# Performance work log

Hardware: AMD Instinct MI355X
Metric: run time of the kernel (lower is better)

## Reference

```python
import jax, jax.numpy as jnp
import numpy as np
import math

B, S, DIM, H = 2, 2048, 1024, 16
Q_DIM = 64                 # cfg.pair_dim
V_DIM = Q_DIM * 3 // 2     # 96
MAX_POS = 2048             # cfg.rope_max_position
EPS = 1e-8
SOFTCAP = 5.0


def apply_rope(x):
    # x: [B, S, H, D]; faithful to torch version: freq = 1/logspace(0, log10(max_pos), D//2)
    D = x.shape[-1]
    nf = D // 2
    freq = 1.0 / jnp.logspace(0.0, math.log10(MAX_POS), nf, dtype=x.dtype)   # [nf]
    positions = jnp.arange(x.shape[1], dtype=x.dtype)                         # [S]
    theta = positions[:, None] * freq                                         # [S, nf]
    sin_t = jnp.sin(theta)[None, :, None, :]                                  # [1,S,1,nf]
    cos_t = jnp.cos(theta)[None, :, None, :]
    x1 = x[..., ::2]
    x2 = x[..., 1::2]
    return jnp.concatenate([x1 * cos_t - x2 * sin_t, x1 * sin_t + x2 * cos_t], axis=-1)


def setup_inputs() -> dict:
    key = jax.random.key(0)
    ks = jax.random.split(key, 9)
    x = jax.random.normal(ks[0], (B, S, DIM), dtype=jnp.float32)
    attention_bias = jax.random.normal(ks[1], (B, H, S, S), dtype=jnp.float32)
    rms_weight = jnp.ones((DIM,), dtype=jnp.float32)
    sd = 1.0 / math.sqrt(DIM)
    Wq = jax.random.normal(ks[2], (DIM, H * Q_DIM), dtype=jnp.float32) * sd
    Wk = jax.random.normal(ks[3], (DIM, Q_DIM), dtype=jnp.float32) * sd
    Wv = jax.random.normal(ks[4], (DIM, V_DIM), dtype=jnp.float32) * sd
    bv = jax.random.normal(ks[5], (V_DIM,), dtype=jnp.float32) * sd
    Wo = jax.random.normal(ks[6], (H * V_DIM, DIM), dtype=jnp.float32) / math.sqrt(H * V_DIM)
    bo = jax.random.normal(ks[7], (DIM,), dtype=jnp.float32) * sd
    return {"x": x, "attention_bias": attention_bias, "rms_weight": rms_weight,
            "Wq": Wq, "Wk": Wk, "Wv": Wv, "bv": bv, "Wo": Wo, "bo": bo}


def reference(x, attention_bias, rms_weight, Wq, Wk, Wv, bv, Wo, bo):
    # RMSNorm
    xn = x * rms_weight / jnp.sqrt(jnp.mean(x * x, axis=-1, keepdims=True) + EPS)
    # projections (MQA: single shared k and v head)
    q = (xn @ Wq).reshape(B, S, H, Q_DIM)          # [B,S,H,Dq]
    k = xn @ Wk                                     # [B,S,Dq]
    v = xn @ Wv + bv                                # [B,S,Dv]
    # RoPE
    q = apply_rope(q)
    k = apply_rope(k[:, :, None, :])[:, :, 0, :]
    # attention logits with tanh soft-cap and external bias: [B,H,S,S]
    logits = jnp.einsum('bihd,bjd->bhij', q, k)
    logits = jnp.tanh((logits + attention_bias) / SOFTCAP) * SOFTCAP
    attn = jax.nn.softmax(logits, axis=-1)
    # context: shared V across heads
    ctx = jnp.einsum('bhij,bjd->bihd', attn, v).reshape(B, S, H * V_DIM)
    return ctx @ Wo + bo
```

## Files before the change

kernel.cpp:

```cpp
#include <hip/hip_runtime.h>
#include <math.h>

#define B_   2
#define S_   2048
#define DIM_ 1024
#define H_   16
#define QD_  64
#define VD_  96
#define NQKV 1184
#define EPS_ 1e-8f

using half_t = _Float16;
using half8  = __attribute__((ext_vector_type(8))) _Float16;
using half4v = __attribute__((ext_vector_type(4))) _Float16;
using f32x4  = __attribute__((ext_vector_type(4))) float;

__global__ __launch_bounds__(256) void rmsnorm_h(const float* __restrict__ x,
                                                 const float* __restrict__ w,
                                                 half_t* __restrict__ xn) {
    int row = blockIdx.x;
    int t = threadIdx.x;
    float4 v = ((const float4*)(x + (size_t)row * DIM_))[t];
    float ss = v.x * v.x + v.y * v.y + v.z * v.z + v.w * v.w;
#pragma unroll
    for (int off = 32; off > 0; off >>= 1) ss += __shfl_down(ss, off, 64);
    __shared__ float wsum[4];
    if ((t & 63) == 0) wsum[t >> 6] = ss;
    __syncthreads();
    float tot = wsum[0] + wsum[1] + wsum[2] + wsum[3];
    float scale = rsqrtf(tot * (1.0f / DIM_) + EPS_);
    float4 wv = ((const float4*)w)[t];
    half4v o;
    o[0] = (half_t)(v.x * wv.x * scale);
    o[1] = (half_t)(v.y * wv.y * scale);
    o[2] = (half_t)(v.z * wv.z * scale);
    o[3] = (half_t)(v.w * wv.w * scale);
    ((half4v*)(xn + (size_t)row * DIM_))[t] = o;
}

template <typename TIN>
__global__ __launch_bounds__(256) void transpose_cvt(const TIN* __restrict__ in,
                                                     half_t* __restrict__ out,
                                                     int R, int C, int ldin,
                                                     size_t zin, size_t zout) {
    __shared__ float tile[32][33];
    in += (size_t)blockIdx.z * zin;
    out += (size_t)blockIdx.z * zout;
    int tx = threadIdx.x & 31, ty = threadIdx.x >> 5;
#pragma unroll
    for (int i = 0; i < 32; i += 8) {
        int r = blockIdx.y * 32 + ty + i, c = blockIdx.x * 32 + tx;
        tile[ty + i][tx] = (float)in[(size_t)r * ldin + c];
    }
    __syncthreads();
#pragma unroll
    for (int i = 0; i < 32; i += 8) {
        int orow = blockIdx.x * 32 + ty + i, ocol = blockIdx.y * 32 + tx;
        out[(size_t)orow * R + ocol] = (half_t)tile[tx][ty + i];
    }
}

__global__ __launch_bounds__(256) void fill_qkv_bias(const float* __restrict__ bv,
                                                     float* __restrict__ bq) {
    int i = blockIdx.x * 256 + threadIdx.x;
    if (i < NQKV) bq[i] = (i >= H_ * QD_ + QD_) ? bv[i - (H_ * QD_ + QD_)] : 0.0f;
}

template <typename OutT, bool BIAS>
__global__ __launch_bounds__(256) void gemm_h(const half_t* __restrict__ A,
                                              const half_t* __restrict__ BT,
                                              OutT* __restrict__ C,
                                              const float* __restrict__ bias,
                                              int M, int N, int K) {
    __shared__ half_t As[128][40];
    __shared__ half_t Bs[128][40];
    int t = threadIdx.x;
    int w = t >> 6, lane = t & 63, l15 = lane & 15, l4 = lane >> 4;
    int wm = (w >> 1) * 64, wn = (w & 1) * 64;
    int m0 = blockIdx.y * 128, n0 = blockIdx.x * 128;
    int r0 = t >> 2, off0 = (t & 3) * 8;
    f32x4 acc[4][4] = {};
    const half8 hz = {};

    const half_t* Ap0 = A + (size_t)(m0 + r0) * K + off0;
    const half_t* Ap1 = Ap0 + (size_t)64 * K;
    const half_t* Bp0 = BT + (size_t)(n0 + r0) * K + off0;
    const half_t* Bp1 = Bp0 + (size_t)64 * K;
    bool bok0 = (n0 + r0) < N, bok1 = (n0 + r0 + 64) < N;

    half8 a0 = *(const half8*)Ap0;
    half8 a1 = *(const half8*)Ap1;
    half8 b0 = bok0 ? *(const half8*)Bp0 : hz;
    half8 b1 = bok1 ? *(const half8*)Bp1 : hz;

    for (int k0 = 0; k0 < K; k0 += 32) {
        __syncthreads();
        *(half8*)&As[r0][off0] = a0;
        *(half8*)&As[r0 + 64][off0] = a1;
        *(half8*)&Bs[r0][off0] = b0;
        *(half8*)&Bs[r0 + 64][off0] = b1;
        __syncthreads();
        if (k0 + 32 < K) {
            a0 = *(const half8*)(Ap0 + k0 + 32);
            a1 = *(const half8*)(Ap1 + k0 + 32);
            b0 = bok0 ? *(const half8*)(Bp0 + k0 + 32) : hz;
            b1 = bok1 ? *(const half8*)(Bp1 + k0 + 32) : hz;
        }
        half8 af[4], bf[4];
#pragma unroll
        for (int mt = 0; mt < 4; ++mt) af[mt] = *(const half8*)&As[wm + mt * 16 + l15][l4 * 8];
#pragma unroll
        for (int nt = 0; nt < 4; ++nt) bf[nt] = *(const half8*)&Bs[wn + nt * 16 + l15][l4 * 8];
#pragma unroll
        for (int mt = 0; mt < 4; ++mt)
#pragma unroll
            for (int nt = 0; nt < 4; ++nt)
                acc[mt][nt] =
                    __builtin_amdgcn_mfma_f32_16x16x32_f16(af[mt], bf[nt], acc[mt][nt], 0, 0, 0);
    }

#pragma unroll
    for (int mt = 0; mt < 4; ++mt)
#pragma unroll
        for (int nt = 0; nt < 4; ++nt) {
            int n = n0 + wn + nt * 16 + l15;
            if (n < N) {
#pragma unroll
                for (int reg = 0; reg < 4; ++reg) {
                    int m = m0 + wm + mt * 16 + l4 * 4 + reg;
                    float v = acc[mt][nt][reg];
                    if (BIAS) v += bias[n];
                    C[(size_t)m * N + n] = (OutT)v;
                }
            }
        }
}

__global__ __launch_bounds__(256) void rope_h(const half_t* __restrict__ in, int ldin,
                                              half_t* __restrict__ out,
                                              int hc, int total_pairs) {
    int p = blockIdx.x * 256 + threadIdx.x;
    if (p >= total_pairs) return;
    int i = p & 31;
    int chunk = p >> 5;
    int row = chunk / hc;
    int h = chunk - row * hc;
    int s = row & (S_ - 1);
    const half_t* src = in + (size_t)row * ldin + h * 64 + 2 * i;
    float x1 = (float)src[0], x2 = (float)src[1];
    float freq = exp2f((float)i * (-11.0f / 31.0f));
    float th = (float)s * freq;
    float sn, cs;
    sincosf(th, &sn, &cs);
    half_t* dst = out + (size_t)chunk * 64;
    dst[i] = (half_t)(x1 * cs - x2 * sn);
    dst[i + 32] = (half_t)(x1 * sn + x2 * cs);
}

__global__ __launch_bounds__(256, 4) void attn_mfma(const half_t* __restrict__ qh,
                                                    const half_t* __restrict__ kh,
                                                    const half_t* __restrict__ vt,
                                                    const float* __restrict__ bias,
                                                    half_t* __restrict__ ctx) {
    __shared__ half_t ks[64][72];
    __shared__ half_t vs[96][72];
    __shared__ half_t ps[4][16][72];

    int t = threadIdx.x;
    int w = t >> 6, lane = t & 63, l15 = lane & 15, l4 = lane >> 4;
    int i0 = blockIdx.x * 64, h = blockIdx.y, b = blockIdx.z;

    const half_t* qbase =
        qh + (((size_t)(b * S_ + i0 + w * 16 + l15) * H_ + h) << 6) + l4 * 8;
    half8 qf0 = *(const half8*)qbase;
    half8 qf1 = *(const half8*)(qbase + 32);

    f32x4 cacc[6] = {};
    float rsum = 0.f;

    int sr = t >> 3, so = (t & 7) * 8;
    const float* bbase =
        bias + ((size_t)(b * H_ + h) * S_ + i0 + w * 16 + l15) * S_ + l4 * 4;
    const half_t* krow0 = kh + (((size_t)b * S_ + sr) << 6) + so;
    const half_t* krow1 = krow0 + ((size_t)32 << 6);
    const half_t* vrow0 = vt + ((size_t)b * 96 + sr) * S_ + so;
    const half_t* vrow1 = vrow0 + (size_t)32 * S_;
    const half_t* vrow2 = vrow0 + (size_t)64 * S_;

    half8 kr0, kr1, vr0, vr1, vr2;
    f32x4 bc[4], bn[4];

    kr0 = *(const half8*)krow0;
    kr1 = *(const half8*)krow1;
    vr0 = *(const half8*)vrow0;
    vr1 = *(const half8*)vrow1;
    vr2 = *(const half8*)vrow2;
#pragma unroll
    for (int nt = 0; nt < 4; ++nt) bc[nt] = *(const f32x4*)(bbase + nt * 16);

    *(half8*)&ks[sr][so] = kr0;
    *(half8*)&ks[sr + 32][so] = kr1;
    *(half8*)&vs[sr][so] = vr0;
    *(half8*)&vs[sr + 32][so] = vr1;
    *(half8*)&vs[sr + 64][so] = vr2;
    __syncthreads();

    for (int j0 = 0; j0 < S_; j0 += 64) {
        int jn = j0 + 64;
        bool more = jn < S_;

        if (more) {
            kr0 = *(const half8*)(krow0 + ((size_t)jn << 6));
            kr1 = *(const half8*)(krow1 + ((size_t)jn << 6));
            vr0 = *(const half8*)(vrow0 + jn);
            vr1 = *(const half8*)(vrow1 + jn);
            vr2 = *(const half8*)(vrow2 + jn);
#pragma unroll
            for (int nt = 0; nt < 4; ++nt) bn[nt] = *(const f32x4*)(bbase + jn + nt * 16);
        }

#pragma unroll
        for (int hf = 0; hf < 2; ++hf) {
#pragma unroll
            for (int nt = hf * 2; nt < hf * 2 + 2; ++nt) {
                f32x4 s = {};
                half8 kb0 = *(const half8*)&ks[nt * 16 + l15][l4 * 8];
                half8 kb1 = *(const half8*)&ks[nt * 16 + l15][32 + l4 * 8];
                __builtin_amdgcn_s_setprio(1);
                s = __builtin_amdgcn_mfma_f32_16x16x32_f16(kb0, qf0, s, 0, 0, 0);
                s = __builtin_amdgcn_mfma_f32_16x16x32_f16(kb1, qf1, s, 0, 0, 0);
                __builtin_amdgcn_s_setprio(0);
                half4v ph;
#pragma unroll
                for (int reg = 0; reg < 4; ++reg) {
                    float l = s[reg] + bc[nt][reg];
                    float e2 = __expf(0.4f * l);
                    float tnh = 1.0f - 2.0f * __builtin_amdgcn_rcpf(e2 + 1.0f);
                    float p = __expf(5.0f * tnh);
                    rsum += p;
                    ph[reg] = (half_t)p;
                }
                *(half4v*)&ps[w][l15][nt * 16 + l4 * 4] = ph;
            }
            half8 af = *(const half8*)&ps[w][l15][hf * 32 + l4 * 8];
            __builtin_amdgcn_s_setprio(1);
#pragma unroll
            for (int nt = 0; nt < 6; ++nt) {
                half8 vv = *(const half8*)&vs[nt * 16 + l15][hf * 32 + l4 * 8];
                cacc[nt] = __builtin_amdgcn_mfma_f32_16x16x32_f16(af, vv, cacc[nt], 0, 0, 0);
            }
            __builtin_amdgcn_s_setprio(0);
        }

        if (more) {
            __syncthreads();
            *(half8*)&ks[sr][so] = kr0;
            *(half8*)&ks[sr + 32][so] = kr1;
            *(half8*)&vs[sr][so] = vr0;
            *(half8*)&vs[sr + 32][so] = vr1;
            *(half8*)&vs[sr + 64][so] = vr2;
            __syncthreads();
#pragma unroll
            for (int nt = 0; nt < 4; ++nt) bc[nt] = bn[nt];
        }
    }

    rsum += __shfl_xor(rsum, 16, 64);
    rsum += __shfl_xor(rsum, 32, 64);
    float rinv = __builtin_amdgcn_rcpf(rsum);
    float rr[4];
#pragma unroll
    for (int reg = 0; reg < 4; ++reg) rr[reg] = __shfl(rinv, l4 * 4 + reg, 64);

#pragma unroll
    for (int nt = 0; nt < 6; ++nt)
#pragma unroll
        for (int reg = 0; reg < 4; ++reg) {
            int i = i0 + w * 16 + l4 * 4 + reg;
            ctx[((size_t)(b * S_ + i) * H_ + h) * VD_ + nt * 16 + l15] =
                (half_t)(cacc[nt][reg] * rr[reg]);
        }
}

extern "C" void kernel_launch(void* const* d_in, const int* in_sizes, int n_in,
                              void* d_out, int out_size, void* d_ws, size_t ws_size,
                              hipStream_t stream) {
    (void)in_sizes; (void)n_in; (void)out_size; (void)ws_size;
    const float* x  = (const float*)d_in[0];
    const float* ab = (const float*)d_in[1];
    const float* rw = (const float*)d_in[2];
    const float* Wq = (const float*)d_in[3];
    const float* Wk = (const float*)d_in[4];
    const float* Wv = (const float*)d_in[5];
    const float* bv = (const float*)d_in[6];
    const float* Wo = (const float*)d_in[7];
    const float* bo = (const float*)d_in[8];
    float* out = (float*)d_out;

    const size_t R = (size_t)B_ * S_;
    half_t* p = (half_t*)d_ws;
    half_t* xn_h  = p;  p += R * DIM_;
    half_t* qkv_h = p;  p += R * NQKV;
    half_t* q_h   = p;  p += R * DIM_;
    half_t* k_h   = p;  p += R * QD_;
    half_t* vtb   = p;  p += R * VD_;
    half_t* ctx_h = p;  p += R * H_ * VD_;
    half_t* WqkvT = p;  p += (size_t)NQKV * DIM_;
    half_t* WoT   = p;  p += (size_t)(H_ * VD_) * DIM_;
    float*  bqkv  = (float*)p;  p += 2 * NQKV;

    rmsnorm_h<<<dim3(R), 256, 0, stream>>>(x, rw, xn_h);

    half_t* WqT = WqkvT;
    half_t* WkT = WqkvT + (size_t)(H_ * QD_) * DIM_;
    half_t* WvT = WkT + (size_t)QD_ * DIM_;
    transpose_cvt<float><<<dim3(32, 32, 1), 256, 0, stream>>>(Wq, WqT, DIM_, H_ * QD_,
                                                              H_ * QD_, 0, 0);
    transpose_cvt<float><<<dim3(2, 32, 1), 256, 0, stream>>>(Wk, WkT, DIM_, QD_, QD_, 0, 0);
    transpose_cvt<float><<<dim3(3, 32, 1), 256, 0, stream>>>(Wv, WvT, DIM_, VD_, VD_, 0, 0);
    transpose_cvt<float><<<dim3(32, 48, 1), 256, 0, stream>>>(Wo, WoT, H_ * VD_, DIM_,
                                                              DIM_, 0, 0);
    fill_qkv_bias<<<dim3((NQKV + 255) / 256), 256, 0, stream>>>(bv, bqkv);

    gemm_h<half_t, true><<<dim3(10, 32), 256, 0, stream>>>(xn_h, WqkvT, qkv_h, bqkv,
                                                           (int)R, NQKV, DIM_);

    rope_h<<<dim3((R * H_ * 32) / 256), 256, 0, stream>>>(qkv_h, NQKV, q_h, H_,
                                                          (int)(R * H_ * 32));
    rope_h<<<dim3((R * 32) / 256), 256, 0, stream>>>(qkv_h + H_ * QD_, NQKV, k_h, 1,
                                                     (int)(R * 32));

    transpose_cvt<half_t><<<dim3(3, 64, 2), 256, 0, stream>>>(
        qkv_h + H_ * QD_ + QD_, vtb, S_, VD_, NQKV, (size_t)S_ * NQKV, (size_t)VD_ * S_);

    attn_mfma<<<dim3(S_ / 64, H_, B_), 256, 0, stream>>>(q_h, k_h, vtb, ab, ctx_h);

    gemm_h<float, true><<<dim3(8, 32), 256, 0, stream>>>(ctx_h, WoT, out, bo,
                                                         (int)R, DIM_, H_ * VD_);
}
```

Measured before the change: 842.2 us.

## Simplify softcap-softmax math, use nontemporal bias loads, halve GEMM M-tile

The tanh soft-cap followed by exp is rewritten algebraically as exp2(-C2/(exp2(C1*s + C1*bias)+1)). The constant factor of exp(5) is dropped, which cancels in the softmax normalisation. This cuts one transcendental and some multiplies per logit, and the bias is pre-scaled when loaded. Bias loads become nontemporal to avoid polluting cache with the large streamed tensor. QK score computation for all four tiles is hoisted ahead of the PV MFMAs, with one priority region around them. The GEMM block tile is shrunk from 128 to 64 rows so twice as many blocks launch, trading per-block reuse for occupancy and grid size.

```diff
diff --git a/kernel.cpp b/kernel.cpp
--- a/kernel.cpp
+++ b/kernel.cpp
@@ -72,47 +72,43 @@
                                               OutT* __restrict__ C,
                                               const float* __restrict__ bias,
                                               int M, int N, int K) {
-    __shared__ half_t As[128][40];
+    __shared__ half_t As[64][40];
     __shared__ half_t Bs[128][40];
     int t = threadIdx.x;
     int w = t >> 6, lane = t & 63, l15 = lane & 15, l4 = lane >> 4;
-    int wm = (w >> 1) * 64, wn = (w & 1) * 64;
-    int m0 = blockIdx.y * 128, n0 = blockIdx.x * 128;
+    int wm = (w >> 1) * 32, wn = (w & 1) * 64;
+    int m0 = blockIdx.y * 64, n0 = blockIdx.x * 128;
     int r0 = t >> 2, off0 = (t & 3) * 8;
-    f32x4 acc[4][4] = {};
+    f32x4 acc[2][4] = {};
     const half8 hz = {};
 
-    const half_t* Ap0 = A + (size_t)(m0 + r0) * K + off0;
-    const half_t* Ap1 = Ap0 + (size_t)64 * K;
+    const half_t* Ap = A + (size_t)(m0 + r0) * K + off0;
     const half_t* Bp0 = BT + (size_t)(n0 + r0) * K + off0;
     const half_t* Bp1 = Bp0 + (size_t)64 * K;
     bool bok0 = (n0 + r0) < N, bok1 = (n0 + r0 + 64) < N;
 
-    half8 a0 = *(const half8*)Ap0;
-    half8 a1 = *(const half8*)Ap1;
+    half8 a0 = *(const half8*)Ap;
     half8 b0 = bok0 ? *(const half8*)Bp0 : hz;
     half8 b1 = bok1 ? *(const half8*)Bp1 : hz;
 
     for (int k0 = 0; k0 < K; k0 += 32) {
         __syncthreads();
         *(half8*)&As[r0][off0] = a0;
-        *(half8*)&As[r0 + 64][off0] = a1;
         *(half8*)&Bs[r0][off0] = b0;
         *(half8*)&Bs[r0 + 64][off0] = b1;
         __syncthreads();
         if (k0 + 32 < K) {
-            a0 = *(const half8*)(Ap0 + k0 + 32);
-            a1 = *(const half8*)(Ap1 + k0 + 32);
+            a0 = *(const half8*)(Ap + k0 + 32);
             b0 = bok0 ? *(const half8*)(Bp0 + k0 + 32) : hz;
             b1 = bok1 ? *(const half8*)(Bp1 + k0 + 32) : hz;
         }
-        half8 af[4], bf[4];
-#pragma unroll
-        for (int mt = 0; mt < 4; ++mt) af[mt] = *(const half8*)&As[wm + mt * 16 + l15][l4 * 8];
+        half8 af[2], bf[4];
+#pragma unroll
+        for (int mt = 0; mt < 2; ++mt) af[mt] = *(const half8*)&As[wm + mt * 16 + l15][l4 * 8];
 #pragma unroll
         for (int nt = 0; nt < 4; ++nt) bf[nt] = *(const half8*)&Bs[wn + nt * 16 + l15][l4 * 8];
 #pragma unroll
-        for (int mt = 0; mt < 4; ++mt)
+        for (int mt = 0; mt < 2; ++mt)
 #pragma unroll
             for (int nt = 0; nt < 4; ++nt)
                 acc[mt][nt] =
@@ -120,7 +116,7 @@
     }
 
 #pragma unroll
-    for (int mt = 0; mt < 4; ++mt)
+    for (int mt = 0; mt < 2; ++mt)
 #pragma unroll
         for (int nt = 0; nt < 4; ++nt) {
             int n = n0 + wn + nt * 16 + l15;
@@ -157,6 +153,9 @@
     dst[i + 32] = (half_t)(x1 * sn + x2 * cs);
 }
 
+#define C1_ 0.57707801635558534f
+#define C2_ 14.426950408889634f
+
 __global__ __launch_bounds__(256, 4) void attn_mfma(const half_t* __restrict__ qh,
                                                     const half_t* __restrict__ kh,
                                                     const half_t* __restrict__ vt,
@@ -196,7 +195,11 @@
     vr1 = *(const half8*)vrow1;
     vr2 = *(const half8*)vrow2;
 #pragma unroll
-    for (int nt = 0; nt < 4; ++nt) bc[nt] = *(const f32x4*)(bbase + nt * 16);
+    for (int nt = 0; nt < 4; ++nt) {
+        f32x4 bb = __builtin_nontemporal_load((const f32x4*)(bbase + nt * 16));
+#pragma unroll
+        for (int e = 0; e < 4; ++e) bc[nt][e] = bb[e] * C1_;
+    }
 
     *(half8*)&ks[sr][so] = kr0;
     *(half8*)&ks[sr + 32][so] = kr1;
@@ -216,41 +219,41 @@
             vr1 = *(const half8*)(vrow1 + jn);
             vr2 = *(const half8*)(vrow2 + jn);
 #pragma unroll
-            for (int nt = 0; nt < 4; ++nt) bn[nt] = *(const f32x4*)(bbase + jn + nt * 16);
-        }
-
+            for (int nt = 0; nt < 4; ++nt)
+                bn[nt] = __builtin_nontemporal_load((const f32x4*)(bbase + jn + nt * 16));
+        }
+
+#pragma unroll
+        for (int nt = 0; nt < 4; ++nt) {
+            f32x4 s = {};
+            half8 kb0 = *(const half8*)&ks[nt * 16 + l15][l4 * 8];
+            half8 kb1 = *(const half8*)&ks[nt * 16 + l15][32 + l4 * 8];
+            __builtin_amdgcn_s_setprio(1);
+            s = __builtin_amdgcn_mfma_f32_16x16x32_f16(kb0, qf0, s, 0, 0, 0);
+            s = __builtin_amdgcn_mfma_f32_16x16x32_f16(kb1, qf1, s, 0, 0, 0);
+            __builtin_amdgcn_s_setprio(0);
+            half4v ph;
+#pragma unroll
+            for (int reg = 0; reg < 4; ++reg) {
+                float u = __builtin_amdgcn_exp2f(fmaf(C1_, s[reg], bc[nt][reg]));
+                float p = __builtin_amdgcn_exp2f(-C2_ * __builtin_amdgcn_rcpf(u + 1.0f));
+                rsum += p;
+                ph[reg] = (half_t)p;
+            }
+            *(half4v*)&ps[w][l15][nt * 16 + l4 * 4] = ph;
+        }
+
+        __builtin_amdgcn_s_setprio(1);
 #pragma unroll
         for (int hf = 0; hf < 2; ++hf) {
-#pragma unroll
-            for (int nt = hf * 2; nt < hf * 2 + 2; ++nt) {
-                f32x4 s = {};
-                half8 kb0 = *(const half8*)&ks[nt * 16 + l15][l4 * 8];
-                half8 kb1 = *(const half8*)&ks[nt * 16 + l15][32 + l4 * 8];
-                __builtin_amdgcn_s_setprio(1);
-                s = __builtin_amdgcn_mfma_f32_16x16x32_f16(kb0, qf0, s, 0, 0, 0);
-                s = __builtin_amdgcn_mfma_f32_16x16x32_f16(kb1, qf1, s, 0, 0, 0);
-                __builtin_amdgcn_s_setprio(0);
-                half4v ph;
-#pragma unroll
-                for (int reg = 0; reg < 4; ++reg) {
-                    float l = s[reg] + bc[nt][reg];
-                    float e2 = __expf(0.4f * l);
-                    float tnh = 1.0f - 2.0f * __builtin_amdgcn_rcpf(e2 + 1.0f);
-                    float p = __expf(5.0f * tnh);
-                    rsum += p;
-                    ph[reg] = (half_t)p;
-                }
-                *(half4v*)&ps[w][l15][nt * 16 + l4 * 4] = ph;
-            }
             half8 af = *(const half8*)&ps[w][l15][hf * 32 + l4 * 8];
-            __builtin_amdgcn_s_setprio(1);
 #pragma unroll
             for (int nt = 0; nt < 6; ++nt) {
                 half8 vv = *(const half8*)&vs[nt * 16 + l15][hf * 32 + l4 * 8];
                 cacc[nt] = __builtin_amdgcn_mfma_f32_16x16x32_f16(af, vv, cacc[nt], 0, 0, 0);
             }
-            __builtin_amdgcn_s_setprio(0);
-        }
+        }
+        __builtin_amdgcn_s_setprio(0);
 
         if (more) {
             __syncthreads();
@@ -261,7 +264,9 @@
             *(half8*)&vs[sr + 64][so] = vr2;
             __syncthreads();
 #pragma unroll
-            for (int nt = 0; nt < 4; ++nt) bc[nt] = bn[nt];
+            for (int nt = 0; nt < 4; ++nt)
+#pragma unroll
+                for (int e = 0; e < 4; ++e) bc[nt][e] = bn[nt][e] * C1_;
         }
     }
 
@@ -322,7 +327,7 @@
                                                               DIM_, 0, 0);
     fill_qkv_bias<<<dim3((NQKV + 255) / 256), 256, 0, stream>>>(bv, bqkv);
 
-    gemm_h<half_t, true><<<dim3(10, 32), 256, 0, stream>>>(xn_h, WqkvT, qkv_h, bqkv,
+    gemm_h<half_t, true><<<dim3(10, 64), 256, 0, stream>>>(xn_h, WqkvT, qkv_h, bqkv,
                                                            (int)R, NQKV, DIM_);
 
     rope_h<<<dim3((R * H_ * 32) / 256), 256, 0, stream>>>(qkv_h, NQKV, q_h, H_,
@@ -335,6 +340,6 @@
 
     attn_mfma<<<dim3(S_ / 64, H_, B_), 256, 0, stream>>>(q_h, k_h, vtb, ab, ctx_h);
 
-    gemm_h<float, true><<<dim3(8, 32), 256, 0, stream>>>(ctx_h, WoT, out, bo,
+    gemm_h<float, true><<<dim3(8, 64), 256, 0, stream>>>(ctx_h, WoT, out, bo,
                                                          (int)R, DIM_, H_ * VD_);
 }
```

After: 831.7 us. About the same (-1.2%).
